# Optimization experiments

Hardware: AMD Instinct MI355X
Metric: run time of the kernel (lower is better)

Reference implementation:

```python
import jax, jax.numpy as jnp
import numpy as np

NU = 100000  # num user nodes
NI = 100000  # num item nodes
E = 1600000  # edges per edge type
L = 100000   # labeled edges
H = 128      # hidden_channels
EPS = 1e-12  # F.normalize eps


def sage_conv(x_src, x_dst, edge_index, w_l, b_l, w_r, num_dst):
    """PyG SAGEConv, mean aggregation, normalize=True.
    w_l, w_r: [H, H] stored as [in, out]; lin_r has no bias."""
    src, dst = edge_index[0], edge_index[1]
    msg_sum = jax.ops.segment_sum(x_src[src], dst, num_segments=num_dst)  # [num_dst, H]
    cnt = jax.ops.segment_sum(jnp.ones((src.shape[0],), x_src.dtype), dst, num_segments=num_dst)
    mean = msg_sum / jnp.maximum(cnt, 1.0)[:, None]
    out = mean @ w_l + b_l + x_dst @ w_r
    norm = jnp.sqrt(jnp.sum(out * out, axis=-1, keepdims=True))
    return out / jnp.maximum(norm, EPS)


def setup_inputs() -> dict:
    key = jax.random.key(0)
    ks = jax.random.split(key, 20)
    s = 1.0 / np.sqrt(H)
    d = {
        'emb_user': jax.random.normal(ks[0], (NU, H), jnp.float32),
        'emb_item': jax.random.normal(ks[1], (NI, H), jnp.float32),
        'edge_rates': jax.random.randint(ks[2], (2, E), 0, 100000, jnp.int32),
        'edge_rev': jax.random.randint(ks[3], (2, E), 0, 100000, jnp.int32),
        'edge_label_index': jax.random.randint(ks[4], (2, L), 0, 100000, jnp.int32),
    }
    names = ['w1l_rates', 'w1r_rates', 'w1l_rev', 'w1r_rev',
             'w2l_rates', 'w2r_rates', 'w2l_rev', 'w2r_rev']
    for i, n in enumerate(names):
        d[n] = jax.random.uniform(ks[5 + i], (H, H), jnp.float32, -s, s)
    for i, n in enumerate(['b1_rates', 'b1_rev', 'b2_rates', 'b2_rev']):
        d[n] = jax.random.uniform(ks[13 + i], (H,), jnp.float32, -s, s)
    return d


def reference(emb_user, emb_item, edge_rates, edge_rev, edge_label_index,
              w1l_rates, w1r_rates, w1l_rev, w1r_rev,
              w2l_rates, w2r_rates, w2l_rev, w2r_rev,
              b1_rates, b1_rev, b2_rates, b2_rev):
    xu, xi = emb_user, emb_item
    # layer 1: each node type receives exactly one edge type (HeteroConv mean is identity)
    xi1 = sage_conv(xu, xi, edge_rates, w1l_rates, b1_rates, w1r_rates, NI)
    xu1 = sage_conv(xi, xu, edge_rev, w1l_rev, b1_rev, w1r_rev, NU)
    xu1 = jax.nn.relu(xu1)  # dropout is identity in eval mode
    xi1 = jax.nn.relu(xi1)
    # layer 2
    xi2 = sage_conv(xu1, xi1, edge_rates, w2l_rates, b2_rates, w2r_rates, NI)
    xu2 = sage_conv(xi1, xu1, edge_rev, w2l_rev, b2_rev, w2r_rev, NU)
    xu2 = jax.nn.relu(xu2)
    xi2 = jax.nn.relu(xi2)
    # classifier: dot(user[src], item[dst])
    x_src = xu2[edge_label_index[0]]
    x_dst = xi2[edge_label_index[1]]
    return jnp.sum(x_src * x_dst, axis=-1)
```

## Files before the change

### kernel.cpp

```cpp
#include <hip/hip_runtime.h>
#include <hip/hip_bf16.h>

#define NUM_U 100000
#define NUM_I 100000
#define NE    1600000
#define NL    100000
#define CAP   48
#define NBIN  391
#define BINCAP 4608
#define ROUND  4096
#define PB    391

typedef __attribute__((ext_vector_type(4))) float floatx4;
typedef __attribute__((ext_vector_type(8))) short shortx8;
typedef unsigned long long u64;

__device__ __forceinline__ float bf_lo(unsigned v) { return __uint_as_float(v << 16); }
__device__ __forceinline__ float bf_hi(unsigned v) { return __uint_as_float(v & 0xffff0000u); }

__device__ __forceinline__ unsigned pack_bf16x2(float lo, float hi) {
    __hip_bfloat16 l = __float2bfloat16(lo);
    __hip_bfloat16 h = __float2bfloat16(hi);
    unsigned short ul = *(unsigned short*)&l;
    unsigned short uh = *(unsigned short*)&h;
    return (unsigned)ul | ((unsigned)uh << 16);
}

__device__ __forceinline__ int clampi(int x, int hi) {
    return min(max(x, 0), hi - 1);
}

__global__ void zero_f32_kernel(float* __restrict__ p, int n) {
    int i = blockIdx.x * blockDim.x + threadIdx.x;
    if (i < n) p[i] = 0.0f;
}

__global__ void conv2_kernel(const float* __restrict__ emb_u, const float* __restrict__ emb_i,
                             unsigned* __restrict__ xu, unsigned* __restrict__ xi) {
    int i = blockIdx.x * blockDim.x + threadIdx.x;
    const int nu = NUM_U * 64;
    if (i < nu) {
        float2 v = ((const float2*)emb_u)[i];
        xu[i] = pack_bf16x2(v.x, v.y);
    } else if (i < nu + NUM_I * 64) {
        int j = i - nu;
        float2 v = ((const float2*)emb_i)[j];
        xi[j] = pack_bf16x2(v.x, v.y);
    }
}

__global__ void transpose_w4_kernel(
    const float* __restrict__ w1l_rates, const float* __restrict__ w1r_rates,
    const float* __restrict__ w1l_rev,   const float* __restrict__ w1r_rev,
    const float* __restrict__ w2l_rates, const float* __restrict__ w2r_rates,
    const float* __restrict__ w2l_rev,   const float* __restrict__ w2r_rev,
    short* __restrict__ Bt, int* __restrict__ bin_cursor) {
    int idx = blockIdx.x * blockDim.x + threadIdx.x;
    if (idx < 2 * NBIN) bin_cursor[idx] = 0;
    int which = idx >> 15;
    int r = idx & 32767;
    int n = r >> 8;
    int k = r & 255;
    const float *wl, *wr;
    switch (which) {
        case 0:  wl = w1l_rates; wr = w1r_rates; break;
        case 1:  wl = w1l_rev;   wr = w1r_rev;   break;
        case 2:  wl = w2l_rates; wr = w2r_rates; break;
        default: wl = w2l_rev;   wr = w2r_rev;   break;
    }
    float v = (k < 128) ? wl[k * 128 + n] : wr[(k - 128) * 128 + n];
    __hip_bfloat16 b = __float2bfloat16(v);
    Bt[idx] = *(const short*)&b;
}

__global__ __launch_bounds__(256) void partition2_kernel(
    const int* __restrict__ edges0, const int* __restrict__ edges1,
    u64* __restrict__ bd0, u64* __restrict__ bd1, int* __restrict__ cur) {
    __shared__ int hist[NBIN];
    __shared__ int prefix[NBIN];
    __shared__ int gbase[NBIN];
    __shared__ __align__(16) u64 sorted[ROUND];

    const int type = (blockIdx.x >= PB) ? 1 : 0;
    const int* edges = type ? edges1 : edges0;
    u64* bin_data = type ? bd1 : bd0;
    int* bin_cursor = cur + type * NBIN;
    const int blk  = blockIdx.x - type * PB;
    const int tid  = threadIdx.x;
    const int lane = tid & 63;
    const int wv   = tid >> 6;
    const int base = blk * ROUND;

    for (int k = tid; k < NBIN; k += 256) hist[k] = 0;
    __syncthreads();

    int mybin[16], myrank[16], mysrc[16], mydst[16];
#pragma unroll
    for (int r = 0; r < 16; r++) {
        int i = base + r * 256 + tid;
        mybin[r] = -1;
        if (i < NE) {
            mysrc[r] = clampi(edges[i], NUM_U);
            mydst[r] = clampi(edges[i + NE], NUM_I);
            mybin[r] = mydst[r] >> 8;
            myrank[r] = atomicAdd(&hist[mybin[r]], 1);
        }
    }
    __syncthreads();

    if (wv == 0) {
        int carry = 0;
        for (int c = 0; c < NBIN; c += 64) {
            int idx = c + lane;
            int h = (idx < NBIN) ? hist[idx] : 0;
            int v = h;
            for (int o = 1; o < 64; o <<= 1) {
                int t = __shfl_up(v, o);
                if (lane >= o) v += t;
            }
            if (idx < NBIN) prefix[idx] = v - h + carry;
            carry += __shfl(v, 63);
        }
    }
    __syncthreads();

#pragma unroll
    for (int r = 0; r < 16; r++) {
        if (mybin[r] >= 0) {
            int j = prefix[mybin[r]] + myrank[r];
            sorted[j] = ((u64)(unsigned)mydst[r] << 32) | (unsigned)mysrc[r];
        }
    }
    __syncthreads();

    for (int b = tid; b < NBIN; b += 256) {
        int cnt = hist[b];
        gbase[b] = (cnt > 0) ? atomicAdd(&bin_cursor[b], cnt) : 0;
    }
    __syncthreads();

    int total = min(ROUND, NE - base);
    for (int j = tid; j < total; j += 256) {
        u64 e = sorted[j];
        int b = (int)(e >> 40);
        int pos = gbase[b] + (j - prefix[b]);
        if (pos < BINCAP)
            bin_data[(size_t)b * BINCAP + pos] = e;
    }
}

__global__ __launch_bounds__(256) void binscatter2_kernel(
    const u64* __restrict__ bd0, const u64* __restrict__ bd1, const int* __restrict__ cur,
    int* __restrict__ deg0, int* __restrict__ bucket0,
    int* __restrict__ deg1, int* __restrict__ bucket1) {
    __shared__ int lbucket[256 * CAP];
    __shared__ int ldeg[256];
    const int type = (blockIdx.x >= NBIN) ? 1 : 0;
    const int b = blockIdx.x - type * NBIN;
    const u64* bin_data = type ? bd1 : bd0;
    int* deg = type ? deg1 : deg0;
    int* bucket = type ? bucket1 : bucket0;
    const int tid = threadIdx.x;
    const int dstbase = b << 8;
    const int n_dst = NUM_I;

    ldeg[tid] = 0;
    __syncthreads();

    int count = min(cur[type * NBIN + b], BINCAP);
    for (int j = tid; j < count; j += 256) {
        u64 e = bin_data[(size_t)b * BINCAP + j];
        int src = (int)(unsigned)e;
        int dl = ((int)(e >> 32)) & 255;
        int pos = atomicAdd(&ldeg[dl], 1);
        if (pos < CAP) lbucket[dl * CAP + pos] = src;
    }
    __syncthreads();

    if (dstbase + tid < n_dst) deg[dstbase + tid] = ldeg[tid];
    int limit = min(256, n_dst - dstbase) * CAP;
    for (int k = tid; k < limit; k += 256)
        bucket[(size_t)dstbase * CAP + k] = lbucket[k];
}

__global__ __launch_bounds__(256) void agg2_kernel(
    const int* __restrict__ degA, const int* __restrict__ bucketA,
    const unsigned* __restrict__ xA, unsigned* __restrict__ outA,
    const int* __restrict__ degB, const int* __restrict__ bucketB,
    const unsigned* __restrict__ xB, unsigned* __restrict__ outB) {
    int w = (blockIdx.x * blockDim.x + threadIdx.x) >> 6;
    int lane = threadIdx.x & 63;
    const int* deg; const int* bucket; const unsigned* xb; unsigned* mo; int node;
    if (w < NUM_I) { deg = degA; bucket = bucketA; xb = xA; mo = outA; node = w; }
    else if (w < NUM_I + NUM_U) { deg = degB; bucket = bucketB; xb = xB; mo = outB; node = w - NUM_I; }
    else return;

    int d = __builtin_nontemporal_load(&deg[node]);
    int cnt = min(d, CAP);
    int srcs = (lane < cnt) ? __builtin_nontemporal_load(&bucket[(size_t)node * CAP + lane]) : 0;
    float a0 = 0.f, a1 = 0.f;
    int e = 0;
    for (; e + 8 <= cnt; e += 8) {
        int s0 = __builtin_amdgcn_readlane(srcs, e + 0);
        int s1 = __builtin_amdgcn_readlane(srcs, e + 1);
        int s2 = __builtin_amdgcn_readlane(srcs, e + 2);
        int s3 = __builtin_amdgcn_readlane(srcs, e + 3);
        int s4 = __builtin_amdgcn_readlane(srcs, e + 4);
        int s5 = __builtin_amdgcn_readlane(srcs, e + 5);
        int s6 = __builtin_amdgcn_readlane(srcs, e + 6);
        int s7 = __builtin_amdgcn_readlane(srcs, e + 7);
        unsigned v0 = xb[(size_t)s0 * 64 + lane];
        unsigned v1 = xb[(size_t)s1 * 64 + lane];
        unsigned v2 = xb[(size_t)s2 * 64 + lane];
        unsigned v3 = xb[(size_t)s3 * 64 + lane];
        unsigned v4 = xb[(size_t)s4 * 64 + lane];
        unsigned v5 = xb[(size_t)s5 * 64 + lane];
        unsigned v6 = xb[(size_t)s6 * 64 + lane];
        unsigned v7 = xb[(size_t)s7 * 64 + lane];
        a0 += bf_lo(v0) + bf_lo(v1) + bf_lo(v2) + bf_lo(v3)
            + bf_lo(v4) + bf_lo(v5) + bf_lo(v6) + bf_lo(v7);
        a1 += bf_hi(v0) + bf_hi(v1) + bf_hi(v2) + bf_hi(v3)
            + bf_hi(v4) + bf_hi(v5) + bf_hi(v6) + bf_hi(v7);
    }
    for (; e + 4 <= cnt; e += 4) {
        int s0 = __builtin_amdgcn_readlane(srcs, e + 0);
        int s1 = __builtin_amdgcn_readlane(srcs, e + 1);
        int s2 = __builtin_amdgcn_readlane(srcs, e + 2);
        int s3 = __builtin_amdgcn_readlane(srcs, e + 3);
        unsigned v0 = xb[(size_t)s0 * 64 + lane];
        unsigned v1 = xb[(size_t)s1 * 64 + lane];
        unsigned v2 = xb[(size_t)s2 * 64 + lane];
        unsigned v3 = xb[(size_t)s3 * 64 + lane];
        a0 += bf_lo(v0) + bf_lo(v1) + bf_lo(v2) + bf_lo(v3);
        a1 += bf_hi(v0) + bf_hi(v1) + bf_hi(v2) + bf_hi(v3);
    }
    for (; e < cnt; e++) {
        int s0 = __builtin_amdgcn_readlane(srcs, e);
        unsigned v0 = xb[(size_t)s0 * 64 + lane];
        a0 += bf_lo(v0); a1 += bf_hi(v0);
    }
    float scale = 1.0f / (float)max(d, 1);
    __builtin_nontemporal_store(pack_bf16x2(a0 * scale, a1 * scale),
                                &mo[(size_t)node * 64 + lane]);
}

__global__ __launch_bounds__(256) void gemm2_kernel(
    const unsigned* __restrict__ meanA, unsigned* __restrict__ xA,
    const short* __restrict__ BtA, const float* __restrict__ biasA,
    const unsigned* __restrict__ meanB, unsigned* __restrict__ xB,
    const short* __restrict__ BtB, const float* __restrict__ biasB,
    int nblocksA) {
    __shared__ __align__(16) short A_lds[128 * 72];
    __shared__ float rowsum[128][2];

    const int half = (blockIdx.x >= nblocksA) ? 1 : 0;
    const unsigned* meanb = half ? meanB : meanA;
    const unsigned* xdstb = half ? xB : xA;
    unsigned* outb = half ? xB : xA;
    const short* Bt = half ? BtB : BtA;
    const float* bias = half ? biasB : biasA;
    const int rb = (blockIdx.x - half * nblocksA) * 128;
    const int n_rows = NUM_I;

    const int tid  = threadIdx.x;
    const int lane = tid & 63;
    const int wv   = tid >> 6;
    const int wm   = wv >> 1;
    const int wn   = wv & 1;
    const int l15  = lane & 15;
    const int lq   = lane >> 4;

    floatx4 acc[4][4];
#pragma unroll
    for (int nt = 0; nt < 4; nt++) {
        float b = bias[wn * 64 + nt * 16 + l15];
#pragma unroll
        for (int mt = 0; mt < 4; mt++) acc[mt][nt] = (floatx4){b, b, b, b};
    }

    for (int kt = 0; kt < 4; kt++) {
        __syncthreads();
        const unsigned* srcbuf = (kt < 2) ? meanb : xdstb;
        const int kbase_u = (kt & 1) * 32;
#pragma unroll
        for (int j = 0; j < 4; j++) {
            int c = tid + j * 256;
            int row = c >> 3;
            int kc = (c & 7) * 8;
            int grow = rb + row;
            uint4 v = make_uint4(0u, 0u, 0u, 0u);
            if (grow < n_rows)
                v = *(const uint4*)(srcbuf + (size_t)grow * 64 + kbase_u + (kc >> 1));
            *(uint4*)&A_lds[row * 72 + kc] = v;
        }
        __syncthreads();

#pragma unroll
        for (int kk = 0; kk < 64; kk += 32) {
            shortx8 af[4], bfr[4];
#pragma unroll
            for (int mt = 0; mt < 4; mt++) {
                int row_l = wm * 64 + mt * 16 + l15;
                af[mt] = *(const shortx8*)&A_lds[row_l * 72 + kk + lq * 8];
            }
#pragma unroll
            for (int nt = 0; nt < 4; nt++) {
                int col = wn * 64 + nt * 16 + l15;
                int kg = kt * 64 + kk + lq * 8;
                bfr[nt] = *(const shortx8*)(Bt + col * 256 + kg);
            }
#pragma unroll
            for (int mt = 0; mt < 4; mt++)
#pragma unroll
                for (int nt = 0; nt < 4; nt++)
                    acc[mt][nt] = __builtin_amdgcn_mfma_f32_16x16x32_bf16(
                        af[mt], bfr[nt], acc[mt][nt], 0, 0, 0);
        }
    }

#pragma unroll
    for (int mt = 0; mt < 4; mt++) {
#pragma unroll
        for (int r = 0; r < 4; r++) {
            float p = 0.f;
#pragma unroll
            for (int nt = 0; nt < 4; nt++) { float x = acc[mt][nt][r]; p += x * x; }
            for (int o = 1; o < 16; o <<= 1) p += __shfl_xor(p, o);
            if (l15 == 0) rowsum[wm * 64 + mt * 16 + lq * 4 + r][wn] = p;
        }
    }
    __syncthreads();

#pragma unroll
    for (int mt = 0; mt < 4; mt++) {
#pragma unroll
        for (int r = 0; r < 4; r++) {
            int row_l = wm * 64 + mt * 16 + lq * 4 + r;
            int grow = rb + row_l;
            float s = rowsum[row_l][0] + rowsum[row_l][1];
            float inv = 1.f / fmaxf(sqrtf(s), 1e-12f);
#pragma unroll
            for (int nt = 0; nt < 4; nt++) {
                float v = fmaxf(acc[mt][nt][r] * inv, 0.f);
                float vnb = __shfl_xor(v, 1);
                if (grow < n_rows && (l15 & 1) == 0) {
                    int colpair = (wn * 64 + nt * 16 + l15) >> 1;
                    outb[(size_t)grow * 64 + colpair] = pack_bf16x2(v, vnb);
                }
            }
        }
    }
}

__global__ __launch_bounds__(256) void classifier_kernel(
    const unsigned* __restrict__ xu, const unsigned* __restrict__ xi,
    const int* __restrict__ eli, float* __restrict__ out, int nL) {
    int wave = (blockIdx.x * blockDim.x + threadIdx.x) >> 6;
    int lane = threadIdx.x & 63;
    if (wave >= nL) return;
    int su = clampi(eli[wave], NUM_U);
    int di = clampi(eli[wave + nL], NUM_I);
    unsigned a = xu[(size_t)su * 64 + lane];
    unsigned b = xi[(size_t)di * 64 + lane];
    float p = bf_lo(a) * bf_lo(b) + bf_hi(a) * bf_hi(b);
    for (int o = 32; o; o >>= 1) p += __shfl_xor(p, o);
    if (lane == 0) __builtin_nontemporal_store(p, &out[wave]);
}

extern "C" void kernel_launch(void* const* d_in, const int* in_sizes, int n_in,
                              void* d_out, int out_size, void* d_ws, size_t ws_size,
                              hipStream_t stream) {
    const float* emb_user = (const float*)d_in[0];
    const float* emb_item = (const float*)d_in[1];
    const int* edge_rates = (const int*)d_in[2];
    const int* edge_rev   = (const int*)d_in[3];
    const int* eli        = (const int*)d_in[4];
    const float* b1_rates = (const float*)d_in[13];
    const float* b1_rev   = (const float*)d_in[14];
    const float* b2_rates = (const float*)d_in[15];
    const float* b2_rev   = (const float*)d_in[16];

    char* p = (char*)d_ws;
    auto alloc = [&](size_t bytes) -> void* {
        void* q = (void*)p;
        p += (bytes + 511) & ~(size_t)511;
        return q;
    };
    int* deg_rates    = (int*)alloc((size_t)NUM_I * 4);
    int* bucket_rates = (int*)alloc((size_t)NUM_I * CAP * 4);
    int* deg_rev      = (int*)alloc((size_t)NUM_U * 4);
    int* bucket_rev   = (int*)alloc((size_t)NUM_U * CAP * 4);
    unsigned* meanI = (unsigned*)alloc((size_t)NUM_I * 64 * 4);
    unsigned* meanU = (unsigned*)alloc((size_t)NUM_U * 64 * 4);
    unsigned* xi    = (unsigned*)alloc((size_t)NUM_I * 64 * 4);
    unsigned* xu    = (unsigned*)alloc((size_t)NUM_U * 64 * 4);
    short* Bt = (short*)alloc((size_t)4 * 32768 * 2);
    int* bin_cursor = (int*)alloc((size_t)2 * NBIN * 4);
    u64* bd0 = (u64*)meanI;
    u64* bd1 = (u64*)meanU;

    const int gemmBlocks = (NUM_I + 127) / 128;
    const int agg2Blocks = ((NUM_I + NUM_U) * 64 + 255) / 256;
    const int conv2Blocks = ((NUM_U + NUM_I) * 64 + 255) / 256;

    if (out_size > NL) {
        int tail = out_size - NL;
        zero_f32_kernel<<<(tail + 255) / 256, 256, 0, stream>>>((float*)d_out + NL, tail);
    }

    transpose_w4_kernel<<<512, 256, 0, stream>>>(
        (const float*)d_in[5], (const float*)d_in[6],
        (const float*)d_in[7], (const float*)d_in[8],
        (const float*)d_in[9], (const float*)d_in[10],
        (const float*)d_in[11], (const float*)d_in[12], Bt, bin_cursor);
    conv2_kernel<<<conv2Blocks, 256, 0, stream>>>(emb_user, emb_item, xu, xi);
    partition2_kernel<<<2 * PB, 256, 0, stream>>>(edge_rates, edge_rev, bd0, bd1, bin_cursor);
    binscatter2_kernel<<<2 * NBIN, 256, 0, stream>>>(bd0, bd1, bin_cursor,
                                                     deg_rates, bucket_rates,
                                                     deg_rev, bucket_rev);

    agg2_kernel<<<agg2Blocks, 256, 0, stream>>>(deg_rates, bucket_rates, xu, meanI,
                                                deg_rev, bucket_rev, xi, meanU);
    gemm2_kernel<<<2 * gemmBlocks, 256, 0, stream>>>(meanI, xi, Bt + 0 * 32768, b1_rates,
                                                     meanU, xu, Bt + 1 * 32768, b1_rev,
                                                     gemmBlocks);

    agg2_kernel<<<agg2Blocks, 256, 0, stream>>>(deg_rates, bucket_rates, xu, meanI,
                                                deg_rev, bucket_rev, xi, meanU);
    gemm2_kernel<<<2 * gemmBlocks, 256, 0, stream>>>(meanI, xi, Bt + 2 * 32768, b2_rates,
                                                     meanU, xu, Bt + 3 * 32768, b2_rev,
                                                     gemmBlocks);

    classifier_kernel<<<(NL * 64 + 255) / 256, 256, 0, stream>>>(xu, xi, eli,
                                                                 (float*)d_out, NL);
}
```

Before: 634.9 us.

## Fuse neighbor mean aggregation into the SAGE GEMM kernel via LDS

Measured after the change: 663.1 us. 1.04x slower.

```diff
diff --git a/kernel.cpp b/kernel.cpp
--- a/kernel.cpp
+++ b/kernel.cpp
@@ -10,6 +10,7 @@
 #define BINCAP 4608
 #define ROUND  4096
 #define PB    391
+#define FM    64
 
 typedef __attribute__((ext_vector_type(4))) float floatx4;
 typedef __attribute__((ext_vector_type(8))) short shortx8;
@@ -183,83 +184,28 @@
         bucket[(size_t)dstbase * CAP + k] = lbucket[k];
 }
 
-__global__ __launch_bounds__(256) void agg2_kernel(
+__global__ __launch_bounds__(256) void fused_kernel(
     const int* __restrict__ degA, const int* __restrict__ bucketA,
-    const unsigned* __restrict__ xA, unsigned* __restrict__ outA,
+    const unsigned* __restrict__ xsA, const unsigned* __restrict__ xdA,
+    const short* __restrict__ BtA, const float* __restrict__ biasA,
+    unsigned* __restrict__ outA,
     const int* __restrict__ degB, const int* __restrict__ bucketB,
-    const unsigned* __restrict__ xB, unsigned* __restrict__ outB) {
-    int w = (blockIdx.x * blockDim.x + threadIdx.x) >> 6;
-    int lane = threadIdx.x & 63;
-    const int* deg; const int* bucket; const unsigned* xb; unsigned* mo; int node;
-    if (w < NUM_I) { deg = degA; bucket = bucketA; xb = xA; mo = outA; node = w; }
-    else if (w < NUM_I + NUM_U) { deg = degB; bucket = bucketB; xb = xB; mo = outB; node = w - NUM_I; }
-    else return;
-
-    int d = __builtin_nontemporal_load(&deg[node]);
-    int cnt = min(d, CAP);
-    int srcs = (lane < cnt) ? __builtin_nontemporal_load(&bucket[(size_t)node * CAP + lane]) : 0;
-    float a0 = 0.f, a1 = 0.f;
-    int e = 0;
-    for (; e + 8 <= cnt; e += 8) {
-        int s0 = __builtin_amdgcn_readlane(srcs, e + 0);
-        int s1 = __builtin_amdgcn_readlane(srcs, e + 1);
-        int s2 = __builtin_amdgcn_readlane(srcs, e + 2);
-        int s3 = __builtin_amdgcn_readlane(srcs, e + 3);
-        int s4 = __builtin_amdgcn_readlane(srcs, e + 4);
-        int s5 = __builtin_amdgcn_readlane(srcs, e + 5);
-        int s6 = __builtin_amdgcn_readlane(srcs, e + 6);
-        int s7 = __builtin_amdgcn_readlane(srcs, e + 7);
-        unsigned v0 = xb[(size_t)s0 * 64 + lane];
-        unsigned v1 = xb[(size_t)s1 * 64 + lane];
-        unsigned v2 = xb[(size_t)s2 * 64 + lane];
-        unsigned v3 = xb[(size_t)s3 * 64 + lane];
-        unsigned v4 = xb[(size_t)s4 * 64 + lane];
-        unsigned v5 = xb[(size_t)s5 * 64 + lane];
-        unsigned v6 = xb[(size_t)s6 * 64 + lane];
-        unsigned v7 = xb[(size_t)s7 * 64 + lane];
-        a0 += bf_lo(v0) + bf_lo(v1) + bf_lo(v2) + bf_lo(v3)
-            + bf_lo(v4) + bf_lo(v5) + bf_lo(v6) + bf_lo(v7);
-        a1 += bf_hi(v0) + bf_hi(v1) + bf_hi(v2) + bf_hi(v3)
-            + bf_hi(v4) + bf_hi(v5) + bf_hi(v6) + bf_hi(v7);
-    }
-    for (; e + 4 <= cnt; e += 4) {
-        int s0 = __builtin_amdgcn_readlane(srcs, e + 0);
-        int s1 = __builtin_amdgcn_readlane(srcs, e + 1);
-        int s2 = __builtin_amdgcn_readlane(srcs, e + 2);
-        int s3 = __builtin_amdgcn_readlane(srcs, e + 3);
-        unsigned v0 = xb[(size_t)s0 * 64 + lane];
-        unsigned v1 = xb[(size_t)s1 * 64 + lane];
-        unsigned v2 = xb[(size_t)s2 * 64 + lane];
-        unsigned v3 = xb[(size_t)s3 * 64 + lane];
-        a0 += bf_lo(v0) + bf_lo(v1) + bf_lo(v2) + bf_lo(v3);
-        a1 += bf_hi(v0) + bf_hi(v1) + bf_hi(v2) + bf_hi(v3);
-    }
-    for (; e < cnt; e++) {
-        int s0 = __builtin_amdgcn_readlane(srcs, e);
-        unsigned v0 = xb[(size_t)s0 * 64 + lane];
-        a0 += bf_lo(v0); a1 += bf_hi(v0);
-    }
-    float scale = 1.0f / (float)max(d, 1);
-    __builtin_nontemporal_store(pack_bf16x2(a0 * scale, a1 * scale),
-                                &mo[(size_t)node * 64 + lane]);
-}
-
-__global__ __launch_bounds__(256) void gemm2_kernel(
-    const unsigned* __restrict__ meanA, unsigned* __restrict__ xA,
-    const short* __restrict__ BtA, const float* __restrict__ biasA,
-    const unsigned* __restrict__ meanB, unsigned* __restrict__ xB,
+    const unsigned* __restrict__ xsB, const unsigned* __restrict__ xdB,
     const short* __restrict__ BtB, const float* __restrict__ biasB,
-    int nblocksA) {
-    __shared__ __align__(16) short A_lds[128 * 72];
-    __shared__ float rowsum[128][2];
+    unsigned* __restrict__ outB, int nblocksA) {
+    __shared__ unsigned mean_lds[FM][68];
+    __shared__ __align__(16) short A_lds[FM * 72];
+    __shared__ float rowsum[FM][2];
 
     const int half = (blockIdx.x >= nblocksA) ? 1 : 0;
-    const unsigned* meanb = half ? meanB : meanA;
-    const unsigned* xdstb = half ? xB : xA;
-    unsigned* outb = half ? xB : xA;
+    const int* deg = half ? degB : degA;
+    const int* bucket = half ? bucketB : bucketA;
+    const unsigned* xsrc = half ? xsB : xsA;
+    const unsigned* xdst = half ? xdB : xdA;
     const short* Bt = half ? BtB : BtA;
     const float* bias = half ? biasB : biasA;
-    const int rb = (blockIdx.x - half * nblocksA) * 128;
+    unsigned* outb = half ? outB : outA;
+    const int rb = (blockIdx.x - half * nblocksA) * FM;
     const int n_rows = NUM_I;
 
     const int tid  = threadIdx.x;
@@ -270,37 +216,125 @@
     const int l15  = lane & 15;
     const int lq   = lane >> 4;
 
-    floatx4 acc[4][4];
+    {
+        const int r0 = rb + wv * 16;
+        int dv = 0;
+        if (lane < 16 && r0 + lane < n_rows)
+            dv = __builtin_nontemporal_load(&deg[r0 + lane]);
+        int srcs = 0;
+        if (r0 < n_rows && lane < CAP)
+            srcs = __builtin_nontemporal_load(&bucket[(size_t)r0 * CAP + lane]);
+        for (int i = 0; i < 16; i++) {
+            const int row = r0 + i;
+            int srcs_next = 0;
+            if (i < 15 && row + 1 < n_rows && lane < CAP)
+                srcs_next = __builtin_nontemporal_load(&bucket[(size_t)(row + 1) * CAP + lane]);
+            int d = __builtin_amdgcn_readlane(dv, i);
+            int cnt = (row < n_rows) ? min(d, CAP) : 0;
+            float a0 = 0.f, a1 = 0.f;
+            int e = 0;
+            for (; e + 8 <= cnt; e += 8) {
+                int s0 = __builtin_amdgcn_readlane(srcs, e + 0);
+                int s1 = __builtin_amdgcn_readlane(srcs, e + 1);
+                int s2 = __builtin_amdgcn_readlane(srcs, e + 2);
+                int s3 = __builtin_amdgcn_readlane(srcs, e + 3);
+                int s4 = __builtin_amdgcn_readlane(srcs, e + 4);
+                int s5 = __builtin_amdgcn_readlane(srcs, e + 5);
+                int s6 = __builtin_amdgcn_readlane(srcs, e + 6);
+                int s7 = __builtin_amdgcn_readlane(srcs, e + 7);
+                unsigned v0 = xsrc[(size_t)s0 * 64 + lane];
+                unsigned v1 = xsrc[(size_t)s1 * 64 + lane];
+                unsigned v2 = xsrc[(size_t)s2 * 64 + lane];
+                unsigned v3 = xsrc[(size_t)s3 * 64 + lane];
+                unsigned v4 = xsrc[(size_t)s4 * 64 + lane];
+                unsigned v5 = xsrc[(size_t)s5 * 64 + lane];
+                unsigned v6 = xsrc[(size_t)s6 * 64 + lane];
+                unsigned v7 = xsrc[(size_t)s7 * 64 + lane];
+                a0 += bf_lo(v0) + bf_lo(v1) + bf_lo(v2) + bf_lo(v3)
+                    + bf_lo(v4) + bf_lo(v5) + bf_lo(v6) + bf_lo(v7);
+                a1 += bf_hi(v0) + bf_hi(v1) + bf_hi(v2) + bf_hi(v3)
+                    + bf_hi(v4) + bf_hi(v5) + bf_hi(v6) + bf_hi(v7);
+            }
+            for (; e + 4 <= cnt; e += 4) {
+                int s0 = __builtin_amdgcn_readlane(srcs, e + 0);
+                int s1 = __builtin_amdgcn_readlane(srcs, e + 1);
+                int s2 = __builtin_amdgcn_readlane(srcs, e + 2);
+                int s3 = __builtin_amdgcn_readlane(srcs, e + 3);
+                unsigned v0 = xsrc[(size_t)s0 * 64 + lane];
+                unsigned v1 = xsrc[(size_t)s1 * 64 + lane];
+                unsigned v2 = xsrc[(size_t)s2 * 64 + lane];
+                unsigned v3 = xsrc[(size_t)s3 * 64 + lane];
+                a0 += bf_lo(v0) + bf_lo(v1) + bf_lo(v2) + bf_lo(v3);
+                a1 += bf_hi(v0) + bf_hi(v1) + bf_hi(v2) + bf_hi(v3);
+            }
+            for (; e < cnt; e++) {
+                int s0 = __builtin_amdgcn_readlane(srcs, e);
+                unsigned v0 = xsrc[(size_t)s0 * 64 + lane];
+                a0 += bf_lo(v0); a1 += bf_hi(v0);
+            }
+            float scale = 1.0f / (float)max(d, 1);
+            if (row < n_rows)
+                mean_lds[row - rb][lane] = pack_bf16x2(a0 * scale, a1 * scale);
+            srcs = srcs_next;
+        }
+    }
+
+    floatx4 acc[2][4];
 #pragma unroll
     for (int nt = 0; nt < 4; nt++) {
         float b = bias[wn * 64 + nt * 16 + l15];
 #pragma unroll
-        for (int mt = 0; mt < 4; mt++) acc[mt][nt] = (floatx4){b, b, b, b};
-    }
-
-    for (int kt = 0; kt < 4; kt++) {
+        for (int mt = 0; mt < 2; mt++) acc[mt][nt] = (floatx4){b, b, b, b};
+    }
+
+    __syncthreads();
+
+#pragma unroll
+    for (int kt = 0; kt < 2; kt++) {
+#pragma unroll
+        for (int kk = 0; kk < 64; kk += 32) {
+            shortx8 af[2], bfr[4];
+#pragma unroll
+            for (int mt = 0; mt < 2; mt++) {
+                int row_l = wm * 32 + mt * 16 + l15;
+                af[mt] = *(const shortx8*)&mean_lds[row_l][kt * 32 + (kk >> 1) + lq * 4];
+            }
+#pragma unroll
+            for (int nt = 0; nt < 4; nt++) {
+                int col = wn * 64 + nt * 16 + l15;
+                int kg = kt * 64 + kk + lq * 8;
+                bfr[nt] = *(const shortx8*)(Bt + col * 256 + kg);
+            }
+#pragma unroll
+            for (int mt = 0; mt < 2; mt++)
+#pragma unroll
+                for (int nt = 0; nt < 4; nt++)
+                    acc[mt][nt] = __builtin_amdgcn_mfma_f32_16x16x32_bf16(
+                        af[mt], bfr[nt], acc[mt][nt], 0, 0, 0);
+        }
+    }
+
+    for (int kt = 2; kt < 4; kt++) {
         __syncthreads();
-        const unsigned* srcbuf = (kt < 2) ? meanb : xdstb;
-        const int kbase_u = (kt & 1) * 32;
-#pragma unroll
-        for (int j = 0; j < 4; j++) {
+#pragma unroll
+        for (int j = 0; j < 2; j++) {
             int c = tid + j * 256;
             int row = c >> 3;
             int kc = (c & 7) * 8;
             int grow = rb + row;
             uint4 v = make_uint4(0u, 0u, 0u, 0u);
             if (grow < n_rows)
-                v = *(const uint4*)(srcbuf + (size_t)grow * 64 + kbase_u + (kc >> 1));
+                v = *(const uint4*)(xdst + (size_t)grow * 64 + (kt - 2) * 32 + (kc >> 1));
             *(uint4*)&A_lds[row * 72 + kc] = v;
         }
         __syncthreads();
 
 #pragma unroll
         for (int kk = 0; kk < 64; kk += 32) {
-            shortx8 af[4], bfr[4];
-#pragma unroll
-            for (int mt = 0; mt < 4; mt++) {
-                int row_l = wm * 64 + mt * 16 + l15;
+            shortx8 af[2], bfr[4];
+#pragma unroll
+            for (int mt = 0; mt < 2; mt++) {
+                int row_l = wm * 32 + mt * 16 + l15;
                 af[mt] = *(const shortx8*)&A_lds[row_l * 72 + kk + lq * 8];
             }
 #pragma unroll
@@ -310,7 +344,7 @@
                 bfr[nt] = *(const shortx8*)(Bt + col * 256 + kg);
             }
 #pragma unroll
-            for (int mt = 0; mt < 4; mt++)
+            for (int mt = 0; mt < 2; mt++)
 #pragma unroll
                 for (int nt = 0; nt < 4; nt++)
                     acc[mt][nt] = __builtin_amdgcn_mfma_f32_16x16x32_bf16(
@@ -319,23 +353,23 @@
     }
 
 #pragma unroll
-    for (int mt = 0; mt < 4; mt++) {
+    for (int mt = 0; mt < 2; mt++) {
 #pragma unroll
         for (int r = 0; r < 4; r++) {
             float p = 0.f;
 #pragma unroll
             for (int nt = 0; nt < 4; nt++) { float x = acc[mt][nt][r]; p += x * x; }
             for (int o = 1; o < 16; o <<= 1) p += __shfl_xor(p, o);
-            if (l15 == 0) rowsum[wm * 64 + mt * 16 + lq * 4 + r][wn] = p;
-        }
-    }
-    __syncthreads();
-
-#pragma unroll
-    for (int mt = 0; mt < 4; mt++) {
+            if (l15 == 0) rowsum[wm * 32 + mt * 16 + lq * 4 + r][wn] = p;
+        }
+    }
+    __syncthreads();
+
+#pragma unroll
+    for (int mt = 0; mt < 2; mt++) {
 #pragma unroll
         for (int r = 0; r < 4; r++) {
-            int row_l = wm * 64 + mt * 16 + lq * 4 + r;
+            int row_l = wm * 32 + mt * 16 + lq * 4 + r;
             int grow = rb + row_l;
             float s = rowsum[row_l][0] + rowsum[row_l][1];
             float inv = 1.f / fmaxf(sqrtf(s), 1e-12f);
@@ -345,7 +379,8 @@
                 float vnb = __shfl_xor(v, 1);
                 if (grow < n_rows && (l15 & 1) == 0) {
                     int colpair = (wn * 64 + nt * 16 + l15) >> 1;
-                    outb[(size_t)grow * 64 + colpair] = pack_bf16x2(v, vnb);
+                    __builtin_nontemporal_store(pack_bf16x2(v, vnb),
+                                                &outb[(size_t)grow * 64 + colpair]);
                 }
             }
         }
@@ -390,17 +425,16 @@
     int* bucket_rates = (int*)alloc((size_t)NUM_I * CAP * 4);
     int* deg_rev      = (int*)alloc((size_t)NUM_U * 4);
     int* bucket_rev   = (int*)alloc((size_t)NUM_U * CAP * 4);
-    unsigned* meanI = (unsigned*)alloc((size_t)NUM_I * 64 * 4);
-    unsigned* meanU = (unsigned*)alloc((size_t)NUM_U * 64 * 4);
-    unsigned* xi    = (unsigned*)alloc((size_t)NUM_I * 64 * 4);
-    unsigned* xu    = (unsigned*)alloc((size_t)NUM_U * 64 * 4);
+    unsigned* xi0 = (unsigned*)alloc((size_t)NUM_I * 64 * 4);
+    unsigned* xu0 = (unsigned*)alloc((size_t)NUM_U * 64 * 4);
+    unsigned* xi1 = (unsigned*)alloc((size_t)NUM_I * 64 * 4);
+    unsigned* xu1 = (unsigned*)alloc((size_t)NUM_U * 64 * 4);
     short* Bt = (short*)alloc((size_t)4 * 32768 * 2);
     int* bin_cursor = (int*)alloc((size_t)2 * NBIN * 4);
-    u64* bd0 = (u64*)meanI;
-    u64* bd1 = (u64*)meanU;
-
-    const int gemmBlocks = (NUM_I + 127) / 128;
-    const int agg2Blocks = ((NUM_I + NUM_U) * 64 + 255) / 256;
+    u64* bd0 = (u64*)xi1;
+    u64* bd1 = (u64*)xu1;
+
+    const int fmBlocks = (NUM_I + FM - 1) / FM;
     const int conv2Blocks = ((NUM_U + NUM_I) * 64 + 255) / 256;
 
     if (out_size > NL) {
@@ -413,24 +447,22 @@
         (const float*)d_in[7], (const float*)d_in[8],
         (const float*)d_in[9], (const float*)d_in[10],
         (const float*)d_in[11], (const float*)d_in[12], Bt, bin_cursor);
-    conv2_kernel<<<conv2Blocks, 256, 0, stream>>>(emb_user, emb_item, xu, xi);
+    conv2_kernel<<<conv2Blocks, 256, 0, stream>>>(emb_user, emb_item, xu0, xi0);
     partition2_kernel<<<2 * PB, 256, 0, stream>>>(edge_rates, edge_rev, bd0, bd1, bin_cursor);
     binscatter2_kernel<<<2 * NBIN, 256, 0, stream>>>(bd0, bd1, bin_cursor,
                                                      deg_rates, bucket_rates,
                                                      deg_rev, bucket_rev);
 
-    agg2_kernel<<<agg2Blocks, 256, 0, stream>>>(deg_rates, bucket_rates, xu, meanI,
-                                                deg_rev, bucket_rev, xi, meanU);
-    gemm2_kernel<<<2 * gemmBlocks, 256, 0, stream>>>(meanI, xi, Bt + 0 * 32768, b1_rates,
-                                                     meanU, xu, Bt + 1 * 32768, b1_rev,
-                                                     gemmBlocks);
-
-    agg2_kernel<<<agg2Blocks, 256, 0, stream>>>(deg_rates, bucket_rates, xu, meanI,
-                                                deg_rev, bucket_rev, xi, meanU);
-    gemm2_kernel<<<2 * gemmBlocks, 256, 0, stream>>>(meanI, xi, Bt + 2 * 32768, b2_rates,
-                                                     meanU, xu, Bt + 3 * 32768, b2_rev,
-                                                     gemmBlocks);
-
-    classifier_kernel<<<(NL * 64 + 255) / 256, 256, 0, stream>>>(xu, xi, eli,
+    fused_kernel<<<2 * fmBlocks, 256, 0, stream>>>(
+        deg_rates, bucket_rates, xu0, xi0, Bt + 0 * 32768, b1_rates, xi1,
+        deg_rev,   bucket_rev,   xi0, xu0, Bt + 1 * 32768, b1_rev,   xu1,
+        fmBlocks);
+
+    fused_kernel<<<2 * fmBlocks, 256, 0, stream>>>(
+        deg_rates, bucket_rates, xu1, xi1, Bt + 2 * 32768, b2_rates, xi0,
+        deg_rev,   bucket_rev,   xi1, xu1, Bt + 3 * 32768, b2_rev,   xu0,
+        fmBlocks);
+
+    classifier_kernel<<<(NL * 64 + 255) / 256, 256, 0, stream>>>(xu0, xi0, eli,
                                                                  (float*)d_out, NL);
 }
```
